# Performance work log

Hardware: AMD Instinct MI355X
Metric: run time of the kernel (lower is better)

## Reference

```python
import jax, jax.numpy as jnp
import numpy as np


def _conv2d(x, w, b):
    # x: [B,C,H,W], w: [O,I,kh,kw] (SAME padding, stride 1)
    y = jax.lax.conv_general_dilated(x, w, (1, 1), 'SAME',
                                     dimension_numbers=('NCHW', 'OIHW', 'NCHW'))
    return y + b[None, :, None, None]


def _conv1x1(x, w, b):
    # w: [O,C], b: [O]
    return jnp.einsum('oc,bchw->bohw', w, x) + b[None, :, None, None]


def _attention(xq, xkv, w, b):
    # w: [3,C,C] (q,k,v), b: [3,C]. Tokens = spatial positions, features = channels.
    B, C, H, W = xq.shape
    q = _conv1x1(xq, w[0], b[0]).reshape(B, C, H * W).transpose(0, 2, 1)   # [B,HW,C]
    k = _conv1x1(xkv, w[1], b[1]).reshape(B, C, H * W).transpose(0, 2, 1)
    v = _conv1x1(xkv, w[2], b[2]).reshape(B, C, H * W).transpose(0, 2, 1)
    scale = 1.0 / jnp.sqrt(jnp.asarray(C, xq.dtype))  # d_k = channels
    a = jax.nn.softmax(jnp.einsum('bnc,bmc->bnm', q, k) * scale, axis=-1)  # [B,HW,HW]
    out = jnp.einsum('bnm,bmc->bnc', a, v).transpose(0, 2, 1).reshape(B, C, H, W)
    return out + xq


def _cell(x, h, c, w, b):
    gates = _conv2d(jnp.concatenate([x, h], axis=1), w, b)
    i, f, o, g = jnp.split(gates, 4, axis=1)
    i, f, o, g = jax.nn.sigmoid(i), jax.nn.sigmoid(f), jax.nn.sigmoid(o), jnp.tanh(g)
    c_new = f * c + i * g
    h_new = o * jnp.tanh(c_new)
    return h_new, c_new


def setup_inputs() -> dict:
    key = jax.random.key(0)
    ks = iter(jax.random.split(key, 32))
    B, T, Cin, H, W = 2, 3, 1, 32, 32
    HID, L, K, OUT = 64, 2, 3, 1
    s = 0.02
    d = {
        'x1_seq': jax.random.normal(next(ks), (B, T, Cin, H, W), jnp.float32),
        'x2_seq': jax.random.normal(next(ks), (B, T, Cin, H, W), jnp.float32),
        # ConvLSTM gate convs: layer0 in = Cin+HID, layer1 in = 2*HID, per stream
        'conv1_w0': jax.random.normal(next(ks), (4 * HID, Cin + HID, K, K)) * s,
        'conv1_b0': jnp.zeros((4 * HID,)),
        'conv1_w1': jax.random.normal(next(ks), (4 * HID, 2 * HID, K, K)) * s,
        'conv1_b1': jnp.zeros((4 * HID,)),
        'conv2_w0': jax.random.normal(next(ks), (4 * HID, Cin + HID, K, K)) * s,
        'conv2_b0': jnp.zeros((4 * HID,)),
        'conv2_w1': jax.random.normal(next(ks), (4 * HID, 2 * HID, K, K)) * s,
        'conv2_b1': jnp.zeros((4 * HID,)),
        # attention 1x1 convs, stacked [L, 3(q/k/v), HID, HID]
        'sah_w': jax.random.normal(next(ks), (L, 3, HID, HID)) * s,
        'sah_b': jnp.zeros((L, 3, HID)),
        'sac_w': jax.random.normal(next(ks), (L, 3, HID, HID)) * s,
        'sac_b': jnp.zeros((L, 3, HID)),
        'cah_w': jax.random.normal(next(ks), (L, 3, HID, HID)) * s,
        'cah_b': jnp.zeros((L, 3, HID)),
        'cac_w': jax.random.normal(next(ks), (L, 3, HID, HID)) * s,
        'cac_b': jnp.zeros((L, 3, HID)),
        # decoder
        'dec_w1': jax.random.normal(next(ks), (HID, HID, 3, 3)) * s,
        'dec_b1': jnp.zeros((HID,)),
        'dec_w2': jax.random.normal(next(ks), (OUT, HID, 3, 3)) * s,
        'dec_b2': jnp.zeros((OUT,)),
        'future_steps': 4,
    }
    return d


def reference(x1_seq, x2_seq,
              conv1_w0, conv1_b0, conv1_w1, conv1_b1,
              conv2_w0, conv2_b0, conv2_w1, conv2_b1,
              sah_w, sah_b, sac_w, sac_b, cah_w, cah_b, cac_w, cac_b,
              dec_w1, dec_b1, dec_w2, dec_b2, future_steps):
    B, T, _, H, W = x1_seq.shape
    HID = sah_w.shape[-1]
    L = sah_w.shape[0]
    cw1 = [(conv1_w0, conv1_b0), (conv1_w1, conv1_b1)]
    cw2 = [(conv2_w0, conv2_b0), (conv2_w1, conv2_b1)]

    def decoder(h):
        return _conv2d(jax.nn.relu(_conv2d(h, dec_w1, dec_b1)), dec_w2, dec_b2)

    z = jnp.zeros((B, HID, H, W), x1_seq.dtype)
    h1s, c1s = [z] * L, [z] * L
    h2s, c2s = [z] * L, [z] * L

    def step(x1_t, x2_t, h1s, c1s, h2s, c2s):
        h1s, c1s, h2s, c2s = list(h1s), list(c1s), list(h2s), list(c2s)
        for l in range(L):
            h1, c1 = _cell(x1_t, h1s[l], c1s[l], *cw1[l])
            h2, c2 = _cell(x2_t, h2s[l], c2s[l], *cw2[l])
            h1 = _attention(h1, h1, sah_w[l], sah_b[l])
            c1 = _attention(c1, c1, sac_w[l], sac_b[l])
            h2 = _attention(h2, h2, sah_w[l], sah_b[l])
            c2 = _attention(c2, c2, sac_w[l], sac_b[l])
            tag_h1, tag_c1 = h1, c1
            h1 = _attention(h1, h2, cah_w[l], cah_b[l])
            c1 = _attention(c1, c2, cac_w[l], cac_b[l])
            h2 = _attention(h2, tag_h1, cah_w[l], cah_b[l])
            c2 = _attention(c2, tag_c1, cac_w[l], cac_b[l])
            h1s[l], c1s[l], h2s[l], c2s[l] = h1, c1, h2, c2
            x1_t, x2_t = h1, h2
        return h1s, c1s, h2s, c2s

    warm1, warm2 = [], []
    for t in range(T):
        h1s, c1s, h2s, c2s = step(x1_seq[:, t], x2_seq[:, t], h1s, c1s, h2s, c2s)
        if t < T - 1:
            warm1.append(h1s[-1])
            warm2.append(h2s[-1])
    pred_warm1 = jnp.stack([decoder(h) for h in warm1], axis=1)
    pred_warm2 = jnp.stack([decoder(h) for h in warm2], axis=1)

    preds1, preds2 = [], []
    for _ in range(int(future_steps)):
        p1 = decoder(h1s[-1])
        p2 = decoder(h2s[-1])
        preds1.append(p1)
        preds2.append(p2)
        h1s, c1s, h2s, c2s = step(p1, p2, h1s, c1s, h2s, c2s)
    preds1 = jnp.stack(preds1, axis=1)
    preds2 = jnp.stack(preds2, axis=1)
    return preds1, preds2, pred_warm1, pred_warm2
```

## Files before the change

kernel.cpp:

```cpp
#include <hip/hip_runtime.h>
#include <math.h>

#define BB 2
#define HIDC 64
#define HWN 1024

typedef _Float16 half8 __attribute__((ext_vector_type(8)));
typedef float f32x4 __attribute__((ext_vector_type(4)));

static __device__ __forceinline__ unsigned short f2h_bits(float v) {
  _Float16 h = (_Float16)v;
  return __builtin_bit_cast(unsigned short, h);
}
static __device__ __forceinline__ float h_back(float v) {
  _Float16 h = (_Float16)v;
  return (float)h;
}

struct TWArgs { const float* src[5]; float* dst[5]; int icn9[5]; int osh[5]; };

__global__ __launch_bounds__(256) void transpose_w(TWArgs a) {
  const int arr = blockIdx.y;
  const int icn9 = a.icn9[arr], osh = a.osh[arr];
  const int ocn = 1 << osh;
  const float* s = a.src[arr];
  float* d = a.dst[arr];
  const int n = icn9 << osh;
  for (int i = blockIdx.x * 256 + threadIdx.x; i < n; i += gridDim.x * 256) {
    int oc = i & (ocn - 1), tt = i >> osh;
    d[i] = s[(size_t)oc * icn9 + tt];
  }
}

struct CellArgs {
  const float* x[2]; long xbs;
  const float* h[2]; const float* c[2];
  const float* w[2]; const float* bias[2];
  float* ho[2]; float* co[2];
};

template<int CX>
__global__ __launch_bounds__(512) void cell_kernel(CellArgs a) {
  constexpr int CT = CX + HIDC;
  constexpr int CH = (CT + 1) / 2;
  __shared__ float sIn[CT * 48];
  __shared__ float sGa[256 * 17];
  __shared__ float sGb[256 * 17];
  const int tile = blockIdx.x;
  const int b = blockIdx.y;
  const int st = blockIdx.z;
  const int ty0 = (tile >> 3) << 2, tx0 = (tile & 7) << 2;
  const float* xp = a.x[st] + (size_t)b * a.xbs;
  const float* hp = a.h[st] + (size_t)b * HIDC * HWN;

  for (int idx = threadIdx.x; idx < CT * 36; idx += 512) {
    int ic = idx / 36, pos = idx - ic * 36;
    int iy = pos / 6, ix = pos - iy * 6;
    int gy = ty0 - 1 + iy, gx = tx0 - 1 + ix;
    float v = 0.f;
    if ((unsigned)gy < 32u && (unsigned)gx < 32u) {
      v = (ic < CX) ? xp[ic * HWN + gy * 32 + gx]
                    : hp[(ic - CX) * HWN + gy * 32 + gx];
    }
    sIn[ic * 48 + iy * 8 + ix] = v;
  }
  __syncthreads();

  const int oc = threadIdx.x & 255;
  const int hh = threadIdx.x >> 8;
  const int icb = hh ? CH : 0, ice = hh ? CT : CH;
  float acc[16];
#pragma unroll
  for (int p = 0; p < 16; ++p) acc[p] = 0.f;
  const float* wp = a.w[st];
  for (int ic = icb; ic < ice; ++ic) {
    float w9[9];
#pragma unroll
    for (int t = 0; t < 9; ++t) w9[t] = wp[(ic * 9 + t) * 256 + oc];
    float in[36];
#pragma unroll
    for (int iy = 0; iy < 6; ++iy) {
      float4 v4 = *(const float4*)&sIn[ic * 48 + iy * 8];
      float2 v2 = *(const float2*)&sIn[ic * 48 + iy * 8 + 4];
      in[iy * 6 + 0] = v4.x; in[iy * 6 + 1] = v4.y; in[iy * 6 + 2] = v4.z;
      in[iy * 6 + 3] = v4.w; in[iy * 6 + 4] = v2.x; in[iy * 6 + 5] = v2.y;
    }
#pragma unroll
    for (int ky = 0; ky < 3; ++ky)
#pragma unroll
      for (int kx = 0; kx < 3; ++kx) {
        const float wv = w9[ky * 3 + kx];
#pragma unroll
        for (int py = 0; py < 4; ++py)
#pragma unroll
          for (int px = 0; px < 4; ++px)
            acc[py * 4 + px] += wv * in[(py + ky) * 6 + (px + kx)];
      }
  }
  float* sGh = hh ? sGb : sGa;
#pragma unroll
  for (int p = 0; p < 16; ++p) sGh[oc * 17 + p] = acc[p];
  __syncthreads();

  const float* cp = a.c[st] + (size_t)b * HIDC * HWN;
  float* hop = a.ho[st] + (size_t)b * HIDC * HWN;
  float* cop = a.co[st] + (size_t)b * HIDC * HWN;
  const float* bias = a.bias[st];
  for (int idx = threadIdx.x; idx < HIDC * 16; idx += 512) {
    int hc = idx >> 4, p = idx & 15;
    float gi = sGa[hc * 17 + p]         + sGb[hc * 17 + p]         + bias[hc];
    float gf = sGa[(hc + 64) * 17 + p]  + sGb[(hc + 64) * 17 + p]  + bias[hc + 64];
    float go = sGa[(hc + 128) * 17 + p] + sGb[(hc + 128) * 17 + p] + bias[hc + 128];
    float gg = sGa[(hc + 192) * 17 + p] + sGb[(hc + 192) * 17 + p] + bias[hc + 192];
    gi = 1.f / (1.f + expf(-gi));
    gf = 1.f / (1.f + expf(-gf));
    go = 1.f / (1.f + expf(-go));
    gg = tanhf(gg);
    int off = hc * HWN + (ty0 + (p >> 2)) * 32 + tx0 + (p & 3);
    float cn = gf * cp[off] + gi * gg;
    cop[off] = cn;
    hop[off] = go * tanhf(cn);
  }
}

struct QkvArgs {
  const float* xq[4]; const float* xkv[4];
  const float* w[4]; const float* bias[4];
  unsigned short *Qh, *Ql, *Kh, *Kl, *Vth, *Vtl;
};

__global__ __launch_bounds__(256) void qkv_kernel(QkvArgs a) {
  __shared__ float sWt[64 * 68];
  const int ptile = blockIdx.x, b = blockIdx.y;
  const int attn = blockIdx.z / 3, proj = blockIdx.z % 3;
  const float* x = (proj == 0 ? a.xq[attn] : a.xkv[attn]) + (size_t)b * HIDC * HWN;
  const float* w = a.w[attn] + proj * 64 * 64;
  const float* bias = a.bias[attn] + proj * 64;
  const size_t bb = (size_t)attn * BB + b;
  for (int i = threadIdx.x; i < 4096; i += 256) {
    int o = i >> 6, c = i & 63;
    sWt[c * 68 + o] = w[i];
  }
  __syncthreads();
  const int pq = threadIdx.x & 63, og = threadIdx.x >> 6;
  const int p0 = ptile * 64 + pq;
  float acc[16];
#pragma unroll
  for (int k = 0; k < 16; ++k) acc[k] = bias[og * 16 + k];
  for (int c = 0; c < 64; ++c) {
    float xv = x[c * HWN + p0];
#pragma unroll
    for (int k = 0; k < 16; k += 4) {
      float4 wv = *(const float4*)&sWt[c * 68 + og * 16 + k];
      acc[k+0] += xv * wv.x; acc[k+1] += xv * wv.y;
      acc[k+2] += xv * wv.z; acc[k+3] += xv * wv.w;
    }
  }
  if (proj <= 1) {
    const float sc = (proj == 0) ? 0.125f : 1.f;
    unsigned short* dh = (proj == 0 ? a.Qh : a.Kh) + (bb << 16) + p0 * 64 + og * 16;
    unsigned short* dl = (proj == 0 ? a.Ql : a.Kl) + (bb << 16) + p0 * 64 + og * 16;
#pragma unroll
    for (int k = 0; k < 16; k += 2) {
      float v0 = acc[k] * sc, v1 = acc[k+1] * sc;
      unsigned short h0 = f2h_bits(v0), h1 = f2h_bits(v1);
      *(unsigned int*)&dh[k] = (unsigned int)h0 | ((unsigned int)h1 << 16);
      unsigned short l0 = f2h_bits(v0 - h_back(v0)), l1 = f2h_bits(v1 - h_back(v1));
      *(unsigned int*)&dl[k] = (unsigned int)l0 | ((unsigned int)l1 << 16);
    }
  } else {
    unsigned short* dvh = a.Vth + (bb << 16);
    unsigned short* dvl = a.Vtl + (bb << 16);
#pragma unroll
    for (int k = 0; k < 16; ++k) {
      float v = acc[k];
      dvh[(size_t)(og * 16 + k) * HWN + p0] = f2h_bits(v);
      dvl[(size_t)(og * 16 + k) * HWN + p0] = f2h_bits(v - h_back(v));
    }
  }
}

struct AttnPArgs {
  const unsigned short *Qh, *Ql, *Kh, *Kl, *Vth, *Vtl;
  float* pbuf;
};

__global__ __launch_bounds__(256) void attn_part(AttnPArgs a) {
  __shared__ unsigned short sP[4][2][16][72];
  const int qt = blockIdx.x >> 2, ks = blockIdx.x & 3;
  const int b = blockIdx.y, at = blockIdx.z;
  const size_t bb = (size_t)at * BB + b;
  const int tid = threadIdx.x;
  const int w = tid >> 6, lane = tid & 63;
  const int g = lane >> 4, qc = lane & 15;
  const int swz = (qc & 7) << 3;
  const unsigned short* Qhp = a.Qh + (bb << 16);
  const unsigned short* Qlp = a.Ql + (bb << 16);
  const unsigned short* Khp = a.Kh + (bb << 16);
  const unsigned short* Klp = a.Kl + (bb << 16);
  const unsigned short* Vhp = a.Vth + (bb << 16);
  const unsigned short* Vlp = a.Vtl + (bb << 16);

  const int qrow = qt * 64 + w * 16 + qc;
  const half8 bqh0 = *(const half8*)&Qhp[qrow * 64 + 0  + g * 8];
  const half8 bqh1 = *(const half8*)&Qhp[qrow * 64 + 32 + g * 8];
  const half8 bql0 = *(const half8*)&Qlp[qrow * 64 + 0  + g * 8];
  const half8 bql1 = *(const half8*)&Qlp[qrow * 64 + 32 + g * 8];

  float mrun = -1e30f, lrun = 0.f;
  f32x4 sO[4];
#pragma unroll
  for (int i = 0; i < 4; ++i) sO[i] = (f32x4)0.f;

  for (int kk = 0; kk < 4; ++kk) {
    const int jt = (ks * 4 + kk) * 64;
    f32x4 sS[4];
#pragma unroll
    for (int i = 0; i < 4; ++i) sS[i] = (f32x4)0.f;
#pragma unroll
    for (int sb = 0; sb < 4; ++sb) {
      const int j = jt + sb * 16 + qc;
      const half8 ah0 = *(const half8*)&Khp[j * 64 + 0  + g * 8];
      const half8 ah1 = *(const half8*)&Khp[j * 64 + 32 + g * 8];
      const half8 al0 = *(const half8*)&Klp[j * 64 + 0  + g * 8];
      const half8 al1 = *(const half8*)&Klp[j * 64 + 32 + g * 8];
      f32x4 d = sS[sb];
      d = __builtin_amdgcn_mfma_f32_16x16x32_f16(ah0, bqh0, d, 0, 0, 0);
      d = __builtin_amdgcn_mfma_f32_16x16x32_f16(ah1, bqh1, d, 0, 0, 0);
      d = __builtin_amdgcn_mfma_f32_16x16x32_f16(ah0, bql0, d, 0, 0, 0);
      d = __builtin_amdgcn_mfma_f32_16x16x32_f16(ah1, bql1, d, 0, 0, 0);
      d = __builtin_amdgcn_mfma_f32_16x16x32_f16(al0, bqh0, d, 0, 0, 0);
      d = __builtin_amdgcn_mfma_f32_16x16x32_f16(al1, bqh1, d, 0, 0, 0);
      sS[sb] = d;
    }
    float mt = -1e30f;
#pragma unroll
    for (int sb = 0; sb < 4; ++sb)
#pragma unroll
      for (int r = 0; r < 4; ++r) mt = fmaxf(mt, sS[sb][r]);
    mt = fmaxf(mt, __shfl_xor(mt, 16));
    mt = fmaxf(mt, __shfl_xor(mt, 32));
    const float mn = fmaxf(mrun, mt);
    const float al = __expf(mrun - mn);
    float p[16];
    float ps = 0.f;
#pragma unroll
    for (int sb = 0; sb < 4; ++sb)
#pragma unroll
      for (int r = 0; r < 4; ++r) {
        float e = __expf(sS[sb][r] - mn);
        p[sb * 4 + r] = e; ps += e;
      }
    ps += __shfl_xor(ps, 16);
    ps += __shfl_xor(ps, 32);
    lrun = lrun * al + ps;
    mrun = mn;
#pragma unroll
    for (int i = 0; i < 4; ++i) {
      sO[i][0] *= al; sO[i][1] *= al; sO[i][2] *= al; sO[i][3] *= al;
    }
#pragma unroll
    for (int sb = 0; sb < 4; ++sb)
#pragma unroll
      for (int rp = 0; rp < 4; rp += 2) {
        int j = sb * 16 + g * 4 + rp;
        int js = j ^ swz;
        float v0 = p[sb * 4 + rp], v1 = p[sb * 4 + rp + 1];
        unsigned short h0 = f2h_bits(v0), h1 = f2h_bits(v1);
        *(unsigned int*)&sP[w][0][qc][js] = (unsigned int)h0 | ((unsigned int)h1 << 16);
        unsigned short l0 = f2h_bits(v0 - h_back(v0)), l1 = f2h_bits(v1 - h_back(v1));
        *(unsigned int*)&sP[w][1][qc][js] = (unsigned int)l0 | ((unsigned int)l1 << 16);
      }
    const half8 ph0 = *(const half8*)&sP[w][0][qc][((0 + g) ^ (qc & 7)) * 8];
    const half8 ph1 = *(const half8*)&sP[w][0][qc][((4 + g) ^ (qc & 7)) * 8];
    const half8 pl0 = *(const half8*)&sP[w][1][qc][((0 + g) ^ (qc & 7)) * 8];
    const half8 pl1 = *(const half8*)&sP[w][1][qc][((4 + g) ^ (qc & 7)) * 8];
#pragma unroll
    for (int vs = 0; vs < 4; ++vs) {
      const int vc = vs * 16 + qc;
      const half8 vh0 = *(const half8*)&Vhp[(size_t)vc * HWN + jt + 0  + g * 8];
      const half8 vh1 = *(const half8*)&Vhp[(size_t)vc * HWN + jt + 32 + g * 8];
      const half8 vl0 = *(const half8*)&Vlp[(size_t)vc * HWN + jt + 0  + g * 8];
      const half8 vl1 = *(const half8*)&Vlp[(size_t)vc * HWN + jt + 32 + g * 8];
      f32x4 d = sO[vs];
      d = __builtin_amdgcn_mfma_f32_16x16x32_f16(vh0, ph0, d, 0, 0, 0);
      d = __builtin_amdgcn_mfma_f32_16x16x32_f16(vh1, ph1, d, 0, 0, 0);
      d = __builtin_amdgcn_mfma_f32_16x16x32_f16(vh0, pl0, d, 0, 0, 0);
      d = __builtin_amdgcn_mfma_f32_16x16x32_f16(vh1, pl1, d, 0, 0, 0);
      d = __builtin_amdgcn_mfma_f32_16x16x32_f16(vl0, ph0, d, 0, 0, 0);
      d = __builtin_amdgcn_mfma_f32_16x16x32_f16(vl1, ph1, d, 0, 0, 0);
      sO[vs] = d;
    }
  }
  float* pb = a.pbuf + ((bb * 16 + qt) * 4 + ks) * 4224;
  const int qloc = w * 16 + qc;
#pragma unroll
  for (int vs = 0; vs < 4; ++vs)
#pragma unroll
    for (int r = 0; r < 4; ++r)
      pb[qloc * 64 + vs * 16 + g * 4 + r] = sO[vs][r];
  if (g == 0) {
    pb[4096 + qloc] = mrun;
    pb[4160 + qloc] = lrun;
  }
}

struct AttnMArgs { const float* pbuf; const float* xq[4]; float* out[4]; };

__global__ __launch_bounds__(256) void attn_merge(AttnMArgs a) {
  __shared__ float sW[4][64];
  __shared__ float sL[64];
  const int qt = blockIdx.x, b = blockIdx.y, at = blockIdx.z;
  const float* pb = a.pbuf + (((size_t)at * BB + b) * 16 + qt) * 4 * 4224;
  if (threadIdx.x < 64) {
    int r = threadIdx.x;
    float mm[4];
#pragma unroll
    for (int i = 0; i < 4; ++i) mm[i] = pb[i * 4224 + 4096 + r];
    float M = fmaxf(fmaxf(mm[0], mm[1]), fmaxf(mm[2], mm[3]));
    float L = 0.f;
#pragma unroll
    for (int i = 0; i < 4; ++i) {
      float wv = __expf(mm[i] - M);
      sW[i][r] = wv;
      L += pb[i * 4224 + 4160 + r] * wv;
    }
    sL[r] = L;
  }
  __syncthreads();
  const int c = threadIdx.x >> 2, rg = (threadIdx.x & 3) * 16;
  const float* xq = a.xq[at] + (size_t)b * HIDC * HWN;
  float* op = a.out[at] + (size_t)b * HIDC * HWN;
  const int p0 = qt * 64 + rg;
#pragma unroll
  for (int rr4 = 0; rr4 < 16; rr4 += 4) {
    float rv[4];
#pragma unroll
    for (int k = 0; k < 4; ++k) {
      int r = rg + rr4 + k;
      float acc = 0.f;
#pragma unroll
      for (int i = 0; i < 4; ++i) acc += pb[i * 4224 + r * 64 + c] * sW[i][r];
      rv[k] = acc / sL[r];
    }
    float4 x4 = *(const float4*)&xq[(size_t)c * HWN + p0 + rr4];
    float4 res; res.x = rv[0] + x4.x; res.y = rv[1] + x4.y;
    res.z = rv[2] + x4.z; res.w = rv[3] + x4.w;
    *(float4*)&op[(size_t)c * HWN + p0 + rr4] = res;
  }
}

struct Dec1Args { const float* in[2]; const float* w; const float* b; float* tmp; };

__global__ __launch_bounds__(512) void dec1_kernel(Dec1Args a) {
  __shared__ float sIn[64 * 48];
  __shared__ float sHa[64 * 17];
  __shared__ float sHb[64 * 17];
  const int tile = blockIdx.x, b = blockIdx.y, st = blockIdx.z;
  const int ty0 = (tile >> 3) << 2, tx0 = (tile & 7) << 2;
  const float* ip = a.in[st] + (size_t)b * HIDC * HWN;
  for (int idx = threadIdx.x; idx < 64 * 36; idx += 512) {
    int ic = idx / 36, pos = idx - ic * 36;
    int iy = pos / 6, ix = pos - iy * 6;
    int gy = ty0 - 1 + iy, gx = tx0 - 1 + ix;
    float v = 0.f;
    if ((unsigned)gy < 32u && (unsigned)gx < 32u) v = ip[ic * HWN + gy * 32 + gx];
    sIn[ic * 48 + iy * 8 + ix] = v;
  }
  __syncthreads();
  const int oc = threadIdx.x & 63, ps = (threadIdx.x >> 6) & 3;
  const int hh = threadIdx.x >> 8;
  const int icb = hh * 32, ice = icb + 32;
  float acc0 = 0.f, acc1 = 0.f, acc2 = 0.f, acc3 = 0.f;
  const float* wp = a.w;
  for (int ic = icb; ic < ice; ++ic) {
    float w9[9];
#pragma unroll
    for (int t = 0; t < 9; ++t) w9[t] = wp[(ic * 9 + t) * 64 + oc];
    float in[18];
#pragma unroll
    for (int ry = 0; ry < 3; ++ry) {
      float4 v4 = *(const float4*)&sIn[ic * 48 + (ps + ry) * 8];
      float2 v2 = *(const float2*)&sIn[ic * 48 + (ps + ry) * 8 + 4];
      in[ry*6+0]=v4.x; in[ry*6+1]=v4.y; in[ry*6+2]=v4.z; in[ry*6+3]=v4.w;
      in[ry*6+4]=v2.x; in[ry*6+5]=v2.y;
    }
#pragma unroll
    for (int ky = 0; ky < 3; ++ky)
#pragma unroll
      for (int kx = 0; kx < 3; ++kx) {
        float wv = w9[ky * 3 + kx];
        acc0 += wv * in[ky * 6 + kx + 0];
        acc1 += wv * in[ky * 6 + kx + 1];
        acc2 += wv * in[ky * 6 + kx + 2];
        acc3 += wv * in[ky * 6 + kx + 3];
      }
  }
  float* sH = hh ? sHb : sHa;
  sH[oc * 17 + ps * 4 + 0] = acc0;
  sH[oc * 17 + ps * 4 + 1] = acc1;
  sH[oc * 17 + ps * 4 + 2] = acc2;
  sH[oc * 17 + ps * 4 + 3] = acc3;
  __syncthreads();
  float* dst = a.tmp + ((size_t)st * BB + b) * HIDC * HWN;
  for (int idx = threadIdx.x; idx < 1024; idx += 512) {
    int oc2 = idx >> 4, p = idx & 15;
    float v = sHa[oc2 * 17 + p] + sHb[oc2 * 17 + p] + a.b[oc2];
    v = fmaxf(v, 0.f);
    dst[(size_t)oc2 * HWN + (ty0 + (p >> 2)) * 32 + tx0 + (p & 3)] = v;
  }
}

struct Dec2Args { const float* tmp; const float* w; const float* b;
                  float* dst0; float* dst1; long bstr; };

__global__ __launch_bounds__(256) void dec2_kernel(Dec2Args a) {
  __shared__ float sIn[64 * 48];
  __shared__ float sW[64 * 9];
  const int tile = blockIdx.x, b = blockIdx.y, st = blockIdx.z;
  const int ty0 = (tile >> 3) << 2, tx0 = (tile & 7) << 2;
  const float* ip = a.tmp + ((size_t)st * BB + b) * HIDC * HWN;
  for (int idx = threadIdx.x; idx < 64 * 36; idx += 256) {
    int ic = idx / 36, pos = idx - ic * 36;
    int iy = pos / 6, ix = pos - iy * 6;
    int gy = ty0 - 1 + iy, gx = tx0 - 1 + ix;
    float v = 0.f;
    if ((unsigned)gy < 32u && (unsigned)gx < 32u) v = ip[ic * HWN + gy * 32 + gx];
    sIn[ic * 48 + iy * 8 + ix] = v;
  }
  for (int idx = threadIdx.x; idx < 576; idx += 256) sW[idx] = a.w[idx];
  __syncthreads();
  const int px = threadIdx.x >> 4, icg = threadIdx.x & 15;
  const int py = px >> 2, pxx = px & 3;
  float acc = 0.f;
#pragma unroll
  for (int i = 0; i < 4; ++i) {
    int ic = icg * 4 + i;
    const float* row = &sIn[ic * 48];
    const float* wv = &sW[ic * 9];
#pragma unroll
    for (int ky = 0; ky < 3; ++ky)
#pragma unroll
      for (int kx = 0; kx < 3; ++kx)
        acc += wv[ky * 3 + kx] * row[(py + ky) * 8 + pxx + kx];
  }
#pragma unroll
  for (int d = 1; d < 16; d <<= 1) acc += __shfl_xor(acc, d);
  if (icg == 0) {
    float* d = (st == 0 ? a.dst0 : a.dst1);
    d[(size_t)b * a.bstr + (ty0 + py) * 32 + tx0 + pxx] = acc + a.b[0];
  }
}

extern "C" void kernel_launch(void* const* d_in, const int* in_sizes, int n_in,
                              void* d_out, int out_size, void* d_ws, size_t ws_size,
                              hipStream_t stream) {
  (void)in_sizes; (void)n_in; (void)out_size; (void)ws_size;
  const float* x1_seq = (const float*)d_in[0];
  const float* x2_seq = (const float*)d_in[1];
  const float* c1w[2] = {(const float*)d_in[2], (const float*)d_in[4]};
  const float* c1b[2] = {(const float*)d_in[3], (const float*)d_in[5]};
  const float* c2w[2] = {(const float*)d_in[6], (const float*)d_in[8]};
  const float* c2b[2] = {(const float*)d_in[7], (const float*)d_in[9]};
  const float* sah_w = (const float*)d_in[10]; const float* sah_b = (const float*)d_in[11];
  const float* sac_w = (const float*)d_in[12]; const float* sac_b = (const float*)d_in[13];
  const float* cah_w = (const float*)d_in[14]; const float* cah_b = (const float*)d_in[15];
  const float* cac_w = (const float*)d_in[16]; const float* cac_b = (const float*)d_in[17];
  const float* dw1 = (const float*)d_in[18]; const float* db1 = (const float*)d_in[19];
  const float* dw2 = (const float*)d_in[20]; const float* db2 = (const float*)d_in[21];
  float* out = (float*)d_out;
  float* ws = (float*)d_ws;

  const size_t SPL = (size_t)BB * HIDC * HWN;
  float* h1s = ws;
  float* c1s = h1s + 2 * SPL;
  float* h2s = c1s + 2 * SPL;
  float* c2s = h2s + 2 * SPL;
  float* hc1 = c2s + 2 * SPL;
  float* cc1 = hc1 + SPL;
  float* hc2 = cc1 + SPL;
  float* cc2 = hc2 + SPL;
  float* hs1 = cc2 + SPL;
  float* cs1 = hs1 + SPL;
  float* hs2 = cs1 + SPL;
  float* cs2 = hs2 + SPL;
  float* Qf  = cs2 + SPL;
  float* Kf  = Qf + 4 * SPL;
  float* Vf  = Kf + 4 * SPL;
  unsigned short* Qh = (unsigned short*)Qf;  unsigned short* Ql = Qh + (size_t)8 * 65536;
  unsigned short* Kh = (unsigned short*)Kf;  unsigned short* Kl = Kh + (size_t)8 * 65536;
  unsigned short* Vth = (unsigned short*)Vf; unsigned short* Vtl = Vth + (size_t)8 * 65536;
  float* dtmp = Vf + 4 * SPL;
  float* pbuf = dtmp + 2 * SPL;
  float* wt10 = pbuf + (size_t)4 * BB * 16 * 4 * 4224;
  float* wt11 = wt10 + 585 * 256;
  float* wt20 = wt11 + 1152 * 256;
  float* wt21 = wt20 + 585 * 256;
  float* wtd  = wt21 + 1152 * 256;

  hipMemsetAsync(ws, 0, 8 * SPL * sizeof(float), stream);

  const dim3 blk(256);
  const dim3 blk2(512);

  {
    TWArgs tw;
    tw.src[0] = c1w[0]; tw.dst[0] = wt10; tw.icn9[0] = 585;  tw.osh[0] = 8;
    tw.src[1] = c1w[1]; tw.dst[1] = wt11; tw.icn9[1] = 1152; tw.osh[1] = 8;
    tw.src[2] = c2w[0]; tw.dst[2] = wt20; tw.icn9[2] = 585;  tw.osh[2] = 8;
    tw.src[3] = c2w[1]; tw.dst[3] = wt21; tw.icn9[3] = 1152; tw.osh[3] = 8;
    tw.src[4] = dw1;    tw.dst[4] = wtd;  tw.icn9[4] = 576;  tw.osh[4] = 6;
    transpose_w<<<dim3(32, 5), blk, 0, stream>>>(tw);
  }

  auto attn_stage = [&](const float* q0, const float* q1, const float* q2, const float* q3,
                        const float* k0, const float* k1, const float* k2, const float* k3,
                        const float* wh, const float* bh, const float* wc, const float* bc,
                        float* o0, float* o1, float* o2, float* o3) {
    QkvArgs qa;
    qa.xq[0]=q0; qa.xq[1]=q1; qa.xq[2]=q2; qa.xq[3]=q3;
    qa.xkv[0]=k0; qa.xkv[1]=k1; qa.xkv[2]=k2; qa.xkv[3]=k3;
    qa.w[0]=wh; qa.w[1]=wc; qa.w[2]=wh; qa.w[3]=wc;
    qa.bias[0]=bh; qa.bias[1]=bc; qa.bias[2]=bh; qa.bias[3]=bc;
    qa.Qh=Qh; qa.Ql=Ql; qa.Kh=Kh; qa.Kl=Kl; qa.Vth=Vth; qa.Vtl=Vtl;
    qkv_kernel<<<dim3(16, BB, 12), blk, 0, stream>>>(qa);
    AttnPArgs ap; ap.Qh=Qh; ap.Ql=Ql; ap.Kh=Kh; ap.Kl=Kl; ap.Vth=Vth; ap.Vtl=Vtl;
    ap.pbuf=pbuf;
    attn_part<<<dim3(64, BB, 4), blk, 0, stream>>>(ap);
    AttnMArgs am; am.pbuf=pbuf;
    am.xq[0]=q0; am.xq[1]=q1; am.xq[2]=q2; am.xq[3]=q3;
    am.out[0]=o0; am.out[1]=o1; am.out[2]=o2; am.out[3]=o3;
    attn_merge<<<dim3(16, BB, 4), blk, 0, stream>>>(am);
  };

  auto decode = [&](long off1, long off2, long bstr) {
    Dec1Args d1; d1.in[0] = h1s + SPL; d1.in[1] = h2s + SPL;
    d1.w = wtd; d1.b = db1; d1.tmp = dtmp;
    dec1_kernel<<<dim3(64, BB, 2), blk2, 0, stream>>>(d1);
    Dec2Args d2; d2.tmp = dtmp; d2.w = dw2; d2.b = db2;
    d2.dst0 = out + off1; d2.dst1 = out + off2; d2.bstr = bstr;
    dec2_kernel<<<dim3(64, BB, 2), blk, 0, stream>>>(d2);
  };

  for (int s = 0; s < 6; ++s) {
    const float *x1, *x2; long xbs;
    if (s < 3) { x1 = x1_seq + s * HWN; x2 = x2_seq + s * HWN; xbs = 3 * HWN; }
    else       { x1 = out + (s - 3) * HWN; x2 = out + 8192 + (s - 3) * HWN; xbs = 4 * HWN; }

    for (int l = 0; l < 2; ++l) {
      if (l == 1) { x1 = h1s; x2 = h2s; xbs = (long)HIDC * HWN; }
      CellArgs ca;
      ca.x[0] = x1; ca.x[1] = x2; ca.xbs = xbs;
      ca.h[0] = h1s + l * SPL; ca.h[1] = h2s + l * SPL;
      ca.c[0] = c1s + l * SPL; ca.c[1] = c2s + l * SPL;
      ca.w[0] = (l == 0) ? wt10 : wt11;
      ca.w[1] = (l == 0) ? wt20 : wt21;
      ca.bias[0] = c1b[l]; ca.bias[1] = c2b[l];
      ca.ho[0] = hc1; ca.ho[1] = hc2; ca.co[0] = cc1; ca.co[1] = cc2;
      if (l == 0) cell_kernel<1><<<dim3(64, BB, 2), blk2, 0, stream>>>(ca);
      else        cell_kernel<64><<<dim3(64, BB, 2), blk2, 0, stream>>>(ca);

      attn_stage(hc1, cc1, hc2, cc2,
                 hc1, cc1, hc2, cc2,
                 sah_w + l * 12288, sah_b + l * 192,
                 sac_w + l * 12288, sac_b + l * 192,
                 hs1, cs1, hs2, cs2);
      attn_stage(hs1, cs1, hs2, cs2,
                 hs2, cs2, hs1, cs1,
                 cah_w + l * 12288, cah_b + l * 192,
                 cac_w + l * 12288, cac_b + l * 192,
                 h1s + l * SPL, c1s + l * SPL, h2s + l * SPL, c2s + l * SPL);
    }

    if (s == 0)      decode(16384,        20480,        2048);
    else if (s == 1) decode(16384 + 1024, 20480 + 1024, 2048);
    else             decode((s - 2) * HWN, 8192 + (s - 2) * HWN, 4096);
  }
}
```

Baseline: 2.073 ms.

## Run ConvLSTM gate convolution on MFMA with split-fp16 weights and inputs

Replaces the scalar FP32 direct 3x3 convolution in the LSTM cell with an implicit-GEMM MFMA kernel. Weights are pre-split into fp16 high and low parts and laid out as [shift][oc][128 channels], and input tiles are staged in XOR-swizzled shared memory as hi/lo fp16. Three MFMAs per product (hh, hl, lh) approximate FP32 accuracy. Tiles become 4x8 pixels with 256 threads, so there are half as many blocks, and the cross-thread reduction through shared memory is removed. This adds zero-padding work on the 65-channel layer and a weight-split preprocessing kernel.

```diff
diff --git a/kernel.cpp b/kernel.cpp
--- a/kernel.cpp
+++ b/kernel.cpp
@@ -17,109 +17,138 @@
   return (float)h;
 }
 
-struct TWArgs { const float* src[5]; float* dst[5]; int icn9[5]; int osh[5]; };
+struct TWArgs { const float* src; float* dst; };
 
 __global__ __launch_bounds__(256) void transpose_w(TWArgs a) {
+  const int n = 576 * 64;
+  for (int i = blockIdx.x * 256 + threadIdx.x; i < n; i += gridDim.x * 256) {
+    int oc = i & 63, tt = i >> 6;
+    a.dst[i] = a.src[(size_t)oc * 576 + tt];
+  }
+}
+
+struct WSArgs { const float* src[4]; unsigned short* dh[4]; unsigned short* dl[4]; int ct[4]; };
+
+__global__ __launch_bounds__(256) void wsplit(WSArgs a) {
   const int arr = blockIdx.y;
-  const int icn9 = a.icn9[arr], osh = a.osh[arr];
-  const int ocn = 1 << osh;
   const float* s = a.src[arr];
-  float* d = a.dst[arr];
-  const int n = icn9 << osh;
+  unsigned short* dh = a.dh[arr];
+  unsigned short* dl = a.dl[arr];
+  const int CTc = a.ct[arr];
+  const int n = 9 * 256 * 128;
   for (int i = blockIdx.x * 256 + threadIdx.x; i < n; i += gridDim.x * 256) {
-    int oc = i & (ocn - 1), tt = i >> osh;
-    d[i] = s[(size_t)oc * icn9 + tt];
+    int t = i >> 15;
+    int rem = i & 32767;
+    int oc = rem >> 7, c = rem & 127;
+    float v = (c < CTc) ? s[((size_t)oc * CTc + c) * 9 + t] : 0.f;
+    dh[i] = f2h_bits(v);
+    dl[i] = f2h_bits(v - h_back(v));
   }
 }
 
 struct CellArgs {
   const float* x[2]; long xbs;
   const float* h[2]; const float* c[2];
-  const float* w[2]; const float* bias[2];
+  const unsigned short* wh[2]; const unsigned short* wl[2];
+  const float* bias[2];
   float* ho[2]; float* co[2];
 };
 
 template<int CX>
-__global__ __launch_bounds__(512) void cell_kernel(CellArgs a) {
+__global__ __launch_bounds__(256) void cell_mfma(CellArgs a) {
   constexpr int CT = CX + HIDC;
-  constexpr int CH = (CT + 1) / 2;
-  __shared__ float sIn[CT * 48];
-  __shared__ float sGa[256 * 17];
-  __shared__ float sGb[256 * 17];
+  constexpr int NCHE = (CT + 31) / 32;
+  __shared__ unsigned short sBh[60 * 128];
+  __shared__ unsigned short sBl[60 * 128];
   const int tile = blockIdx.x;
-  const int b = blockIdx.y;
-  const int st = blockIdx.z;
-  const int ty0 = (tile >> 3) << 2, tx0 = (tile & 7) << 2;
+  const int b = blockIdx.y, st = blockIdx.z;
+  const int ty0 = (tile >> 2) * 4, tx0 = (tile & 3) * 8;
   const float* xp = a.x[st] + (size_t)b * a.xbs;
   const float* hp = a.h[st] + (size_t)b * HIDC * HWN;
 
-  for (int idx = threadIdx.x; idx < CT * 36; idx += 512) {
-    int ic = idx / 36, pos = idx - ic * 36;
-    int iy = pos / 6, ix = pos - iy * 6;
-    int gy = ty0 - 1 + iy, gx = tx0 - 1 + ix;
-    float v = 0.f;
-    if ((unsigned)gy < 32u && (unsigned)gx < 32u) {
-      v = (ic < CX) ? xp[ic * HWN + gy * 32 + gx]
-                    : hp[(ic - CX) * HWN + gy * 32 + gx];
-    }
-    sIn[ic * 48 + iy * 8 + ix] = v;
+  for (int j = threadIdx.x; j < 6 * 128; j += 256) {
+    int y = j >> 7, c = j & 127;
+    int gy = ty0 - 1 + y;
+    bool cok = (c < CT) && ((unsigned)gy < 32u);
+    const float* srcp = (c < CX) ? (xp + (size_t)c * HWN)
+                                 : (hp + (size_t)(c < CT ? (c - CX) : 0) * HWN);
+#pragma unroll
+    for (int x = 0; x < 10; ++x) {
+      int gx = tx0 - 1 + x;
+      float v = 0.f;
+      if (cok && (unsigned)gx < 32u) v = srcp[gy * 32 + gx];
+      int row = y * 10 + x;
+      int idx = row * 128 + ((((c >> 3) ^ (row & 7)) << 3) | (c & 7));
+      sBh[idx] = f2h_bits(v);
+      sBl[idx] = f2h_bits(v - h_back(v));
+    }
   }
   __syncthreads();
 
-  const int oc = threadIdx.x & 255;
-  const int hh = threadIdx.x >> 8;
-  const int icb = hh ? CH : 0, ice = hh ? CT : CH;
-  float acc[16];
-#pragma unroll
-  for (int p = 0; p < 16; ++p) acc[p] = 0.f;
-  const float* wp = a.w[st];
-  for (int ic = icb; ic < ice; ++ic) {
-    float w9[9];
-#pragma unroll
-    for (int t = 0; t < 9; ++t) w9[t] = wp[(ic * 9 + t) * 256 + oc];
-    float in[36];
-#pragma unroll
-    for (int iy = 0; iy < 6; ++iy) {
-      float4 v4 = *(const float4*)&sIn[ic * 48 + iy * 8];
-      float2 v2 = *(const float2*)&sIn[ic * 48 + iy * 8 + 4];
-      in[iy * 6 + 0] = v4.x; in[iy * 6 + 1] = v4.y; in[iy * 6 + 2] = v4.z;
-      in[iy * 6 + 3] = v4.w; in[iy * 6 + 4] = v2.x; in[iy * 6 + 5] = v2.y;
-    }
-#pragma unroll
-    for (int ky = 0; ky < 3; ++ky)
-#pragma unroll
-      for (int kx = 0; kx < 3; ++kx) {
-        const float wv = w9[ky * 3 + kx];
-#pragma unroll
-        for (int py = 0; py < 4; ++py)
-#pragma unroll
-          for (int px = 0; px < 4; ++px)
-            acc[py * 4 + px] += wv * in[(py + ky) * 6 + (px + kx)];
+  const int w = threadIdx.x >> 6, lane = threadIdx.x & 63;
+  const int g = lane >> 4, col = lane & 15;
+  f32x4 acc[4][2];
+#pragma unroll
+  for (int gt = 0; gt < 4; ++gt) { acc[gt][0] = (f32x4)0.f; acc[gt][1] = (f32x4)0.f; }
+  const unsigned short* whp = a.wh[st];
+  const unsigned short* wlp = a.wl[st];
+
+  for (int sh = 0; sh < 9; ++sh) {
+    const int ky = sh / 3, kx = sh - ky * 3;
+#pragma unroll
+    for (int ch = 0; ch < NCHE; ++ch) {
+      half8 ahf[4], alf[4];
+#pragma unroll
+      for (int gt = 0; gt < 4; ++gt) {
+        int oc = (gt * 4 + w) * 16 + col;
+        size_t off = (((size_t)sh * 256 + oc) << 7) + ch * 32 + g * 8;
+        ahf[gt] = *(const half8*)&whp[off];
+        alf[gt] = *(const half8*)&wlp[off];
       }
-  }
-  float* sGh = hh ? sGb : sGa;
-#pragma unroll
-  for (int p = 0; p < 16; ++p) sGh[oc * 17 + p] = acc[p];
-  __syncthreads();
+#pragma unroll
+      for (int pt = 0; pt < 2; ++pt) {
+        int py = pt * 2 + (col >> 3), pxx = col & 7;
+        int row = (py + ky) * 10 + pxx + kx;
+        int idx = row * 128 + (((ch * 4 + g) ^ (row & 7)) << 3);
+        half8 bh = *(const half8*)&sBh[idx];
+        half8 bl = *(const half8*)&sBl[idx];
+#pragma unroll
+        for (int gt = 0; gt < 4; ++gt) {
+          f32x4 d = acc[gt][pt];
+          d = __builtin_amdgcn_mfma_f32_16x16x32_f16(ahf[gt], bh, d, 0, 0, 0);
+          d = __builtin_amdgcn_mfma_f32_16x16x32_f16(ahf[gt], bl, d, 0, 0, 0);
+          d = __builtin_amdgcn_mfma_f32_16x16x32_f16(alf[gt], bh, d, 0, 0, 0);
+          acc[gt][pt] = d;
+        }
+      }
+    }
+  }
 
   const float* cp = a.c[st] + (size_t)b * HIDC * HWN;
   float* hop = a.ho[st] + (size_t)b * HIDC * HWN;
   float* cop = a.co[st] + (size_t)b * HIDC * HWN;
   const float* bias = a.bias[st];
-  for (int idx = threadIdx.x; idx < HIDC * 16; idx += 512) {
-    int hc = idx >> 4, p = idx & 15;
-    float gi = sGa[hc * 17 + p]         + sGb[hc * 17 + p]         + bias[hc];
-    float gf = sGa[(hc + 64) * 17 + p]  + sGb[(hc + 64) * 17 + p]  + bias[hc + 64];
-    float go = sGa[(hc + 128) * 17 + p] + sGb[(hc + 128) * 17 + p] + bias[hc + 128];
-    float gg = sGa[(hc + 192) * 17 + p] + sGb[(hc + 192) * 17 + p] + bias[hc + 192];
-    gi = 1.f / (1.f + expf(-gi));
-    gf = 1.f / (1.f + expf(-gf));
-    go = 1.f / (1.f + expf(-go));
-    gg = tanhf(gg);
-    int off = hc * HWN + (ty0 + (p >> 2)) * 32 + tx0 + (p & 3);
-    float cn = gf * cp[off] + gi * gg;
-    cop[off] = cn;
-    hop[off] = go * tanhf(cn);
+#pragma unroll
+  for (int r = 0; r < 4; ++r) {
+    const int hc = w * 16 + g * 4 + r;
+    const float bi = bias[hc], bf = bias[hc + 64];
+    const float bo = bias[hc + 128], bg = bias[hc + 192];
+#pragma unroll
+    for (int pt = 0; pt < 2; ++pt) {
+      float gi = acc[0][pt][r] + bi;
+      float gf = acc[1][pt][r] + bf;
+      float go = acc[2][pt][r] + bo;
+      float gg = acc[3][pt][r] + bg;
+      gi = 1.f / (1.f + expf(-gi));
+      gf = 1.f / (1.f + expf(-gf));
+      go = 1.f / (1.f + expf(-go));
+      gg = tanhf(gg);
+      int py = pt * 2 + (col >> 3), pxx = col & 7;
+      int off = hc * HWN + (ty0 + py) * 32 + tx0 + pxx;
+      float cn = gf * cp[off] + gi * gg;
+      cop[off] = cn;
+      hop[off] = go * tanhf(cn);
+    }
   }
 }
 
@@ -492,11 +521,10 @@
   unsigned short* Vth = (unsigned short*)Vf; unsigned short* Vtl = Vth + (size_t)8 * 65536;
   float* dtmp = Vf + 4 * SPL;
   float* pbuf = dtmp + 2 * SPL;
-  float* wt10 = pbuf + (size_t)4 * BB * 16 * 4 * 4224;
-  float* wt11 = wt10 + 585 * 256;
-  float* wt20 = wt11 + 1152 * 256;
-  float* wt21 = wt20 + 585 * 256;
-  float* wtd  = wt21 + 1152 * 256;
+  float* wsb  = pbuf + (size_t)4 * BB * 16 * 4 * 4224;
+  unsigned short* wsp = (unsigned short*)wsb;
+  const size_t WN = (size_t)9 * 256 * 128;
+  float* wtd = wsb + (8 * WN) / 2;
 
   hipMemsetAsync(ws, 0, 8 * SPL * sizeof(float), stream);
 
@@ -504,13 +532,18 @@
   const dim3 blk2(512);
 
   {
-    TWArgs tw;
-    tw.src[0] = c1w[0]; tw.dst[0] = wt10; tw.icn9[0] = 585;  tw.osh[0] = 8;
-    tw.src[1] = c1w[1]; tw.dst[1] = wt11; tw.icn9[1] = 1152; tw.osh[1] = 8;
-    tw.src[2] = c2w[0]; tw.dst[2] = wt20; tw.icn9[2] = 585;  tw.osh[2] = 8;
-    tw.src[3] = c2w[1]; tw.dst[3] = wt21; tw.icn9[3] = 1152; tw.osh[3] = 8;
-    tw.src[4] = dw1;    tw.dst[4] = wtd;  tw.icn9[4] = 576;  tw.osh[4] = 6;
-    transpose_w<<<dim3(32, 5), blk, 0, stream>>>(tw);
+    TWArgs tw; tw.src = dw1; tw.dst = wtd;
+    transpose_w<<<dim3(32), blk, 0, stream>>>(tw);
+    WSArgs wsa;
+    wsa.src[0] = c1w[0]; wsa.ct[0] = 65;
+    wsa.src[1] = c1w[1]; wsa.ct[1] = 128;
+    wsa.src[2] = c2w[0]; wsa.ct[2] = 65;
+    wsa.src[3] = c2w[1]; wsa.ct[3] = 128;
+    for (int i = 0; i < 4; ++i) {
+      wsa.dh[i] = wsp + i * WN;
+      wsa.dl[i] = wsp + (4 + i) * WN;
+    }
+    wsplit<<<dim3(64, 4), blk, 0, stream>>>(wsa);
   }
 
   auto attn_stage = [&](const float* q0, const float* q1, const float* q2, const float* q3,
@@ -553,12 +586,14 @@
       ca.x[0] = x1; ca.x[1] = x2; ca.xbs = xbs;
       ca.h[0] = h1s + l * SPL; ca.h[1] = h2s + l * SPL;
       ca.c[0] = c1s + l * SPL; ca.c[1] = c2s + l * SPL;
-      ca.w[0] = (l == 0) ? wt10 : wt11;
-      ca.w[1] = (l == 0) ? wt20 : wt21;
+      ca.wh[0] = wsp + (l == 0 ? 0 : 1) * WN;
+      ca.wh[1] = wsp + (l == 0 ? 2 : 3) * WN;
+      ca.wl[0] = wsp + (4 + (l == 0 ? 0 : 1)) * WN;
+      ca.wl[1] = wsp + (4 + (l == 0 ? 2 : 3)) * WN;
       ca.bias[0] = c1b[l]; ca.bias[1] = c2b[l];
       ca.ho[0] = hc1; ca.ho[1] = hc2; ca.co[0] = cc1; ca.co[1] = cc2;
-      if (l == 0) cell_kernel<1><<<dim3(64, BB, 2), blk2, 0, stream>>>(ca);
-      else        cell_kernel<64><<<dim3(64, BB, 2), blk2, 0, stream>>>(ca);
+      if (l == 0) cell_mfma<1><<<dim3(32, BB, 2), blk, 0, stream>>>(ca);
+      else        cell_mfma<64><<<dim3(32, BB, 2), blk, 0, stream>>>(ca);
 
       attn_stage(hc1, cc1, hc2, cc2,
                  hc1, cc1, hc2, cc2,
```

After: 2.107 ms. No clear change (+1.6%).
